# Kernel optimization log

Hardware: AMD Instinct MI355X
Metric: run time of the kernel (lower is better)

## Reference

```python
import jax, jax.numpy as jnp
import numpy as np

N_ITERS = 30  # fixed-iteration surrogate for the data-dependent while-loop power iteration
BN_EPS = 1e-5


def conv1x1(x, w, b):
    # x: [B,C,H,W], w: [O,C], b: [O]
    return jnp.einsum('bchw,oc->bohw', x, w) + b[None, :, None, None]


def bn_relu(x, gamma, beta):
    # training-mode BatchNorm2d (batch statistics over B,H,W per channel) + ReLU
    mean = jnp.mean(x, axis=(0, 2, 3), keepdims=True)
    var = jnp.var(x, axis=(0, 2, 3), keepdims=True)
    xn = (x - mean) * jax.lax.rsqrt(var + BN_EPS)
    return jax.nn.relu(gamma[None, :, None, None] * xn + beta[None, :, None, None])


def power_iteration_u(W, v0):
    # W: [B, N, M]  (N = H*W, M = mid_ch), v0: [B, M]
    # Batched power iteration on W^T W; returns leading left singular vector u: [B, N]
    Ws = jnp.einsum('bnm,bnk->bmk', W, W)  # [B, M, M]

    def step(v, _):
        v = jnp.einsum('bmk,bk->bm', Ws, v)
        v = v / jnp.linalg.norm(v, axis=-1, keepdims=True)
        return v, None

    v, _ = jax.lax.scan(step, v0, None, length=N_ITERS)
    u = jnp.einsum('bnm,bm->bn', W, v)
    u = u / jnp.linalg.norm(u, axis=-1, keepdims=True)
    return u


def setup_inputs() -> dict:
    key = jax.random.key(0)
    B, C, H, W = 32, 64, 128, 128
    M = C // 8  # mid_ch = in_ch // k
    ks = jax.random.split(key, 10)
    he = np.sqrt(2.0 / C).astype(np.float32)
    inp = {
        'x': jax.random.normal(ks[0], (B, C, H, W), dtype=jnp.float32),
        'f_w': jax.random.normal(ks[1], (M, C), dtype=jnp.float32) * he,
        'f_b': jnp.zeros((M,), jnp.float32),
        'f_gamma': jnp.ones((M,), jnp.float32),
        'f_beta': jnp.zeros((M,), jnp.float32),
        'g_w': jax.random.normal(ks[2], (M, C), dtype=jnp.float32) * he,
        'g_b': jnp.zeros((M,), jnp.float32),
        'g_gamma': jnp.ones((M,), jnp.float32),
        'g_beta': jnp.zeros((M,), jnp.float32),
        'h_w': jax.random.normal(ks[3], (M, C), dtype=jnp.float32) * he,
        'h_b': jnp.zeros((M,), jnp.float32),
        'v_w': jax.random.normal(ks[4], (C, M), dtype=jnp.float32) * np.sqrt(2.0 / M).astype(np.float32),
        'v_b': jnp.zeros((C,), jnp.float32),
        'v0f': jax.random.normal(ks[5], (B, M), dtype=jnp.float32),
        'v0g': jax.random.normal(ks[6], (B, M), dtype=jnp.float32),
    }
    return inp


def reference(x, f_w, f_b, f_gamma, f_beta, g_w, g_b, g_gamma, g_beta,
              h_w, h_b, v_w, v_b, v0f, v0g):
    B, C, H, W = x.shape
    M = f_w.shape[0]
    N = H * W
    # f, g: conv1x1 + BN + ReLU; h: conv1x1; all reshaped to [B, N, M]
    fx = bn_relu(conv1x1(x, f_w, f_b), f_gamma, f_beta).reshape(B, M, N).transpose(0, 2, 1)
    gx = bn_relu(conv1x1(x, g_w, g_b), g_gamma, g_beta).reshape(B, M, N).transpose(0, 2, 1)
    hx = conv1x1(x, h_w, h_b).reshape(B, M, N).transpose(0, 2, 1)
    # per-sample leading left singular vectors (batched power iteration)
    uf = power_iteration_u(fx, v0f)  # [B, N]
    ug = power_iteration_u(gx, v0g)  # [B, N]
    # z = u_f @ (u_g^T @ h_x)  -> rank-1 attention, [B, N, M]
    coef = jnp.einsum('bn,bnm->bm', ug, hx)       # [B, M]
    z = uf[:, :, None] * coef[:, None, :]         # [B, N, M]
    z = z.transpose(0, 2, 1).reshape(B, M, H, W)
    z = conv1x1(z, v_w, v_b)
    return z + x
```

## Files before the change

### kernel.cpp

```cpp
#include <hip/hip_runtime.h>

#define BB   32
#define CC   64
#define MM   8
#define NSP  16384
#define CNTF 524288.0f

typedef float f32x4 __attribute__((ext_vector_type(4)));
typedef unsigned int u32x2 __attribute__((ext_vector_type(2)));

#define OFF_FXP_B    0ull
#define OFF_GXP_B    8388608ull
#define OFF_HX_B     16777216ull
#define OFF_PSTATS_B 25165824ull
#define OFF_PWSA_B   (OFF_PSTATS_B + 512ull*32*4)
#define OFF_STATS_B  (OFF_PWSA_B + 32ull*3*8*64*4)

#define AXPY(A, WS, XV) \
    (A).x = fmaf((WS), (XV).x, (A).x); (A).y = fmaf((WS), (XV).y, (A).y); \
    (A).z = fmaf((WS), (XV).z, (A).z); (A).w = fmaf((WS), (XV).w, (A).w);

__device__ __forceinline__ unsigned pk_bf2(float a, float b) {
    unsigned ua = __float_as_uint(a); ua += 0x7FFFu + ((ua >> 16) & 1u);
    unsigned ub = __float_as_uint(b); ub += 0x7FFFu + ((ub >> 16) & 1u);
    return (ua >> 16) | (ub & 0xFFFF0000u);
}
__device__ __forceinline__ float lo16(unsigned u) { return __uint_as_float(u << 16); }
__device__ __forceinline__ float hi16(unsigned u) { return __uint_as_float(u & 0xFFFF0000u); }

__global__ __launch_bounds__(256, 2) void k_conv(const float* __restrict__ x,
        const float* __restrict__ fw, const float* __restrict__ gw,
        const float* __restrict__ hw,
        const float* __restrict__ fb, const float* __restrict__ gb,
        const float* __restrict__ hb, char* __restrict__ wsb) {
    __shared__ float wt[1536];
    __shared__ float sred[4][32];
    for (int i = threadIdx.x; i < 1536; i += 256) {
        int c = i / 24, k = i % 24;
        wt[i] = (k < 8) ? fw[k * 64 + c]
              : (k < 16) ? gw[(k - 8) * 64 + c]
                         : hw[(k - 16) * 64 + c];
    }
    __syncthreads();

    int g  = blockIdx.x * 256 + threadIdx.x;
    int b  = g >> 12;
    int n0 = (g & 4095) * 4;

    const float* xp = x + (size_t)b * CC * NSP + n0;

    float4 af[8], ag[8], ah[8];
#pragma unroll
    for (int m = 0; m < 8; ++m) {
        float bf = fb[m], bg = gb[m], bh = hb[m];
        af[m] = make_float4(bf, bf, bf, bf);
        ag[m] = make_float4(bg, bg, bg, bg);
        ah[m] = make_float4(bh, bh, bh, bh);
    }

#pragma unroll 8
    for (int c = 0; c < 64; ++c) {
        float4 xv = *(const float4*)(xp + (size_t)c * NSP);
        const float4* w4 = (const float4*)(&wt[c * 24]);
        float4 wf0 = w4[0], wf1 = w4[1], wg0 = w4[2], wg1 = w4[3], wh0 = w4[4], wh1 = w4[5];
        AXPY(af[0], wf0.x, xv); AXPY(af[1], wf0.y, xv); AXPY(af[2], wf0.z, xv); AXPY(af[3], wf0.w, xv);
        AXPY(af[4], wf1.x, xv); AXPY(af[5], wf1.y, xv); AXPY(af[6], wf1.z, xv); AXPY(af[7], wf1.w, xv);
        AXPY(ag[0], wg0.x, xv); AXPY(ag[1], wg0.y, xv); AXPY(ag[2], wg0.z, xv); AXPY(ag[3], wg0.w, xv);
        AXPY(ag[4], wg1.x, xv); AXPY(ag[5], wg1.y, xv); AXPY(ag[6], wg1.z, xv); AXPY(ag[7], wg1.w, xv);
        AXPY(ah[0], wh0.x, xv); AXPY(ah[1], wh0.y, xv); AXPY(ah[2], wh0.z, xv); AXPY(ah[3], wh0.w, xv);
        AXPY(ah[4], wh1.x, xv); AXPY(ah[5], wh1.y, xv); AXPY(ah[6], wh1.z, xv); AXPY(ah[7], wh1.w, xv);
    }

    unsigned short* fx16 = (unsigned short*)(wsb + OFF_FXP_B);
    unsigned short* gx16 = (unsigned short*)(wsb + OFF_GXP_B);
    unsigned short* hx16 = (unsigned short*)(wsb + OFF_HX_B);
    size_t base = (size_t)b * MM * NSP + n0;
#pragma unroll
    for (int m = 0; m < 8; ++m) {
        u32x2 pf; pf.x = pk_bf2(af[m].x, af[m].y); pf.y = pk_bf2(af[m].z, af[m].w);
        u32x2 pg; pg.x = pk_bf2(ag[m].x, ag[m].y); pg.y = pk_bf2(ag[m].z, ag[m].w);
        u32x2 ph; ph.x = pk_bf2(ah[m].x, ah[m].y); ph.y = pk_bf2(ah[m].z, ah[m].w);
        *(u32x2*)(fx16 + base + (size_t)m * NSP) = pf;
        *(u32x2*)(gx16 + base + (size_t)m * NSP) = pg;
        *(u32x2*)(hx16 + base + (size_t)m * NSP) = ph;
    }

    int wid = threadIdx.x >> 6, lane = threadIdx.x & 63;
#pragma unroll
    for (int m = 0; m < 8; ++m) {
        float fs = af[m].x + af[m].y + af[m].z + af[m].w;
        float fq = af[m].x * af[m].x + af[m].y * af[m].y + af[m].z * af[m].z + af[m].w * af[m].w;
        float gs = ag[m].x + ag[m].y + ag[m].z + ag[m].w;
        float gq = ag[m].x * ag[m].x + ag[m].y * ag[m].y + ag[m].z * ag[m].z + ag[m].w * ag[m].w;
#pragma unroll
        for (int o = 1; o < 64; o <<= 1) {
            fs += __shfl_xor(fs, o); fq += __shfl_xor(fq, o);
            gs += __shfl_xor(gs, o); gq += __shfl_xor(gq, o);
        }
        if (lane == 0) {
            sred[wid][m] = fs; sred[wid][8 + m] = fq;
            sred[wid][16 + m] = gs; sred[wid][24 + m] = gq;
        }
    }
    __syncthreads();
    if (threadIdx.x < 32) {
        float t = sred[0][threadIdx.x] + sred[1][threadIdx.x]
                + sred[2][threadIdx.x] + sred[3][threadIdx.x];
        ((float*)(wsb + OFF_PSTATS_B))[blockIdx.x * 32 + threadIdx.x] = t;
    }
}

__global__ __launch_bounds__(256) void k_gram(
        const float* __restrict__ fgam, const float* __restrict__ fbet,
        const float* __restrict__ ggam, const float* __restrict__ gbet,
        char* __restrict__ wsb) {
    int bid = blockIdx.x;
    int chunk = bid & 7, which = (bid >> 3) % 3, b = bid / 24;

    __shared__ float sst[8][32];
    __shared__ float stot[32];
    {
        int t32 = threadIdx.x & 31, seg = threadIdx.x >> 5;
        const float* ps = (const float*)(wsb + OFF_PSTATS_B);
        float s = 0.f;
#pragma unroll 8
        for (int i = 0; i < 64; ++i) s += ps[(seg * 64 + i) * 32 + t32];
        sst[seg][t32] = s;
    }
    __syncthreads();
    if (threadIdx.x < 32) {
        float t = 0.f;
#pragma unroll
        for (int w = 0; w < 8; ++w) t += sst[w][threadIdx.x];
        stot[threadIdx.x] = t;
        if (bid == 0) ((float*)(wsb + OFF_STATS_B))[threadIdx.x] = t;
    }
    __syncthreads();

    const float* st  = stot + (which == 0 ? 0 : 16);
    const float* gam = (which == 0) ? fgam : ggam;
    const float* bet = (which == 0) ? fbet : gbet;
    const float inv = 1.f / CNTF;
    float a[8], ccf[8];
#pragma unroll
    for (int m = 0; m < 8; ++m) {
        float mean = st[m] * inv;
        float var  = st[8 + m] * inv - mean * mean;
        float sc   = gam[m] / sqrtf(var + 1e-5f);
        a[m] = sc; ccf[m] = bet[m] - mean * sc;
    }

    const unsigned short* src = (const unsigned short*)
        (wsb + (which == 0 ? OFF_FXP_B : OFF_GXP_B)) + (size_t)b * MM * NSP;
    const unsigned short* hsrc = (const unsigned short*)
        (wsb + OFF_HX_B) + (size_t)b * MM * NSP;

    float acc[64];
#pragma unroll
    for (int j = 0; j < 64; ++j) acc[j] = 0.f;

#pragma unroll
    for (int i = 0; i < 2; ++i) {
        int n = (chunk * 512 + i * 256 + threadIdx.x) * 4;
        float4 vv[8], hh[8];
#pragma unroll
        for (int m = 0; m < 8; ++m) {
            u32x2 u = *(const u32x2*)(src + (size_t)m * NSP + n);
            float4 t;
            t.x = fmaf(a[m], lo16(u.x), ccf[m]); t.x = t.x > 0.f ? t.x : 0.f;
            t.y = fmaf(a[m], hi16(u.x), ccf[m]); t.y = t.y > 0.f ? t.y : 0.f;
            t.z = fmaf(a[m], lo16(u.y), ccf[m]); t.z = t.z > 0.f ? t.z : 0.f;
            t.w = fmaf(a[m], hi16(u.y), ccf[m]); t.w = t.w > 0.f ? t.w : 0.f;
            vv[m] = t;
        }
        if (which == 2) {
#pragma unroll
            for (int m = 0; m < 8; ++m) {
                u32x2 u = *(const u32x2*)(hsrc + (size_t)m * NSP + n);
                hh[m] = make_float4(lo16(u.x), hi16(u.x), lo16(u.y), hi16(u.y));
            }
        } else {
#pragma unroll
            for (int m = 0; m < 8; ++m) hh[m] = vv[m];
        }
#pragma unroll
        for (int m2 = 0; m2 < 8; ++m2)
#pragma unroll
            for (int k = 0; k < 8; ++k) {
                float t = acc[m2 * 8 + k];
                t = fmaf(hh[m2].x, vv[k].x, t);
                t = fmaf(hh[m2].y, vv[k].y, t);
                t = fmaf(hh[m2].z, vv[k].z, t);
                t = fmaf(hh[m2].w, vv[k].w, t);
                acc[m2 * 8 + k] = t;
            }
    }

    int lane = threadIdx.x & 63;
#pragma unroll
    for (int s2 = 0; s2 < 6; ++s2) {
        int half = 32 >> s2;
        int up = (lane >> s2) & 1;
#pragma unroll
        for (int j = 0; j < 32; ++j) {
            if (j >= half) break;
            float send = up ? acc[j] : acc[j + half];
            float recv = __shfl_xor(send, 1 << s2);
            float keep = up ? acc[j + half] : acc[j];
            acc[j] = keep + recv;
        }
    }
    __shared__ float sacc[64];
    if (threadIdx.x < 64) sacc[threadIdx.x] = 0.f;
    __syncthreads();
    int rev = __brev((unsigned)lane) >> 26;
    atomicAdd(&sacc[rev], acc[0]);
    __syncthreads();
    float* pw = (float*)(wsb + OFF_PWSA_B) + (((size_t)b * 3 + which) * 8 + chunk) * 64;
    if (threadIdx.x < 64) pw[threadIdx.x] = sacc[threadIdx.x];
}

__global__ __launch_bounds__(256, 4) void k_out(const float* __restrict__ x,
        const float* __restrict__ fgam, const float* __restrict__ fbet,
        const float* __restrict__ vw, const float* __restrict__ vb,
        const float* __restrict__ v0f, const float* __restrict__ v0g,
        const char* __restrict__ wsb, float* __restrict__ out) {
    int bid = blockIdx.x;
    int b = bid >> 5, sub = bid & 31;
    int tile = sub & 15, ch0 = (sub >> 4) * 32;
    __shared__ float s_vfn[8], s_coef[8], s_w2[64];

    const float* pw = (const float*)(wsb + OFF_PWSA_B) + (size_t)b * 3 * 8 * 64;
    if (threadIdx.x < 16) {
        int grp = threadIdx.x >> 3, m = threadIdx.x & 7;
        float row[8];
#pragma unroll
        for (int k = 0; k < 8; ++k) {
            float s = 0.f;
#pragma unroll
            for (int ch = 0; ch < 8; ++ch) s += pw[(grp * 8 + ch) * 64 + m * 8 + k];
            row[k] = s;
        }
        float v = (grp == 0 ? v0f : v0g)[b * 8 + m];
        for (int it = 0; it < 30; ++it) {
            float t = 0.f;
#pragma unroll
            for (int k = 0; k < 8; ++k) t = fmaf(row[k], __shfl(v, k, 8), t);
            float s = t * t;
            s += __shfl_xor(s, 1, 8); s += __shfl_xor(s, 2, 8); s += __shfl_xor(s, 4, 8);
            v = t / sqrtf(s);
        }
        float t = 0.f;
#pragma unroll
        for (int k = 0; k < 8; ++k) t = fmaf(row[k], __shfl(v, k, 8), t);
        float s = v * t;
        s += __shfl_xor(s, 1, 8); s += __shfl_xor(s, 2, 8); s += __shfl_xor(s, 4, 8);
        float invn = 1.f / sqrtf(s);
        if (grp == 0) {
            s_vfn[m] = v * invn;
        } else {
            float cf = 0.f;
#pragma unroll
            for (int k = 0; k < 8; ++k) {
                float cr = 0.f;
#pragma unroll
                for (int ch = 0; ch < 8; ++ch) cr += pw[(2 * 8 + ch) * 64 + m * 8 + k];
                cf = fmaf(cr, __shfl(v, k, 8), cf);
            }
            s_coef[m] = cf * invn;
        }
    }
    __syncthreads();
    if (threadIdx.x < 64) {
        float acc = 0.f;
#pragma unroll
        for (int k = 0; k < 8; ++k) acc = fmaf(vw[threadIdx.x * 8 + k], s_coef[k], acc);
        s_w2[threadIdx.x] = acc;
    }
    __syncthreads();

    int n0 = tile * 1024 + threadIdx.x * 4;
    const float inv = 1.f / CNTF;
    const float* stats = (const float*)(wsb + OFF_STATS_B);
    const unsigned short* fx16 = (const unsigned short*)(wsb + OFF_FXP_B);

    float uf0 = 0.f, uf1 = 0.f, uf2 = 0.f, uf3 = 0.f;
#pragma unroll
    for (int m = 0; m < 8; ++m) {
        float mean = stats[m] * inv;
        float var  = stats[8 + m] * inv - mean * mean;
        float a    = fgam[m] / sqrtf(var + 1e-5f);
        float cc   = fbet[m] - mean * a;
        float vf   = s_vfn[m];
        u32x2 u = *(const u32x2*)(fx16 + (size_t)(b * 8 + m) * NSP + n0);
        float t0 = fmaf(a, lo16(u.x), cc); t0 = t0 > 0.f ? t0 : 0.f; uf0 = fmaf(vf, t0, uf0);
        float t1 = fmaf(a, hi16(u.x), cc); t1 = t1 > 0.f ? t1 : 0.f; uf1 = fmaf(vf, t1, uf1);
        float t2 = fmaf(a, lo16(u.y), cc); t2 = t2 > 0.f ? t2 : 0.f; uf2 = fmaf(vf, t2, uf2);
        float t3 = fmaf(a, hi16(u.y), cc); t3 = t3 > 0.f ? t3 : 0.f; uf3 = fmaf(vf, t3, uf3);
    }

    const float* xp = x   + (size_t)(b * CC + ch0) * NSP + n0;
    float*       op = out + (size_t)(b * CC + ch0) * NSP + n0;
#pragma unroll 8
    for (int c = 0; c < 32; ++c) {
        float w2c = s_w2[ch0 + c];
        float bc  = vb[ch0 + c];
        float4 xv = *(const float4*)(xp + (size_t)c * NSP);
        f32x4 ov;
        ov.x = fmaf(uf0, w2c, xv.x + bc);
        ov.y = fmaf(uf1, w2c, xv.y + bc);
        ov.z = fmaf(uf2, w2c, xv.z + bc);
        ov.w = fmaf(uf3, w2c, xv.w + bc);
        __builtin_nontemporal_store(ov, (f32x4*)(op + (size_t)c * NSP));
    }
}

extern "C" void kernel_launch(void* const* d_in, const int* in_sizes, int n_in,
                              void* d_out, int out_size, void* d_ws, size_t ws_size,
                              hipStream_t stream) {
    const float* x    = (const float*)d_in[0];
    const float* f_w  = (const float*)d_in[1];
    const float* f_b  = (const float*)d_in[2];
    const float* f_g  = (const float*)d_in[3];
    const float* f_be = (const float*)d_in[4];
    const float* g_w  = (const float*)d_in[5];
    const float* g_b  = (const float*)d_in[6];
    const float* g_g  = (const float*)d_in[7];
    const float* g_be = (const float*)d_in[8];
    const float* h_w  = (const float*)d_in[9];
    const float* h_b  = (const float*)d_in[10];
    const float* v_w  = (const float*)d_in[11];
    const float* v_b  = (const float*)d_in[12];
    const float* v0f  = (const float*)d_in[13];
    const float* v0g  = (const float*)d_in[14];
    char*  wsb = (char*)d_ws;
    float* out = (float*)d_out;

    k_conv<<<512,  256, 0, stream>>>(x, f_w, g_w, h_w, f_b, g_b, h_b, wsb);
    k_gram<<<768,  256, 0, stream>>>(f_g, f_be, g_g, g_be, wsb);
    k_out <<<1024, 256, 0, stream>>>(x, f_g, f_be, v_w, v_b, v0f, v0g, wsb, out);
}
```

Measured before the change: 102.3 us.

## Halve conv per-thread width and move power iteration into separate kernel

Result: slower. 113.1 us (+10.6%).

```diff
diff --git a/kernel.cpp b/kernel.cpp
--- a/kernel.cpp
+++ b/kernel.cpp
@@ -7,18 +7,18 @@
 #define CNTF 524288.0f
 
 typedef float f32x4 __attribute__((ext_vector_type(4)));
+typedef float f32x2 __attribute__((ext_vector_type(2)));
 typedef unsigned int u32x2 __attribute__((ext_vector_type(2)));
 
 #define OFF_FXP_B    0ull
 #define OFF_GXP_B    8388608ull
 #define OFF_HX_B     16777216ull
 #define OFF_PSTATS_B 25165824ull
-#define OFF_PWSA_B   (OFF_PSTATS_B + 512ull*32*4)
+#define OFF_PWSA_B   (OFF_PSTATS_B + 1024ull*32*4)
 #define OFF_STATS_B  (OFF_PWSA_B + 32ull*3*8*64*4)
-
-#define AXPY(A, WS, XV) \
-    (A).x = fmaf((WS), (XV).x, (A).x); (A).y = fmaf((WS), (XV).y, (A).y); \
-    (A).z = fmaf((WS), (XV).z, (A).z); (A).w = fmaf((WS), (XV).w, (A).w);
+#define OFF_COEF_B   (OFF_STATS_B + 32ull*4)
+#define OFF_VFN_B    (OFF_COEF_B + 16ull*4)
+#define OFF_W2_B     (OFF_VFN_B + (unsigned long long)BB*8*4)
 
 __device__ __forceinline__ unsigned pk_bf2(float a, float b) {
     unsigned ua = __float_as_uint(a); ua += 0x7FFFu + ((ua >> 16) & 1u);
@@ -28,7 +28,7 @@
 __device__ __forceinline__ float lo16(unsigned u) { return __uint_as_float(u << 16); }
 __device__ __forceinline__ float hi16(unsigned u) { return __uint_as_float(u & 0xFFFF0000u); }
 
-__global__ __launch_bounds__(256, 2) void k_conv(const float* __restrict__ x,
+__global__ __launch_bounds__(256, 4) void k_conv(const float* __restrict__ x,
         const float* __restrict__ fw, const float* __restrict__ gw,
         const float* __restrict__ hw,
         const float* __restrict__ fb, const float* __restrict__ gb,
@@ -44,31 +44,32 @@
     __syncthreads();
 
     int g  = blockIdx.x * 256 + threadIdx.x;
-    int b  = g >> 12;
-    int n0 = (g & 4095) * 4;
+    int b  = g >> 13;
+    int n0 = (g & 8191) * 2;
 
     const float* xp = x + (size_t)b * CC * NSP + n0;
 
-    float4 af[8], ag[8], ah[8];
-#pragma unroll
-    for (int m = 0; m < 8; ++m) {
-        float bf = fb[m], bg = gb[m], bh = hb[m];
-        af[m] = make_float4(bf, bf, bf, bf);
-        ag[m] = make_float4(bg, bg, bg, bg);
-        ah[m] = make_float4(bh, bh, bh, bh);
+    f32x2 af[8], ag[8], ah[8];
+#pragma unroll
+    for (int m = 0; m < 8; ++m) {
+        af[m].x = af[m].y = fb[m];
+        ag[m].x = ag[m].y = gb[m];
+        ah[m].x = ah[m].y = hb[m];
     }
 
 #pragma unroll 8
     for (int c = 0; c < 64; ++c) {
-        float4 xv = *(const float4*)(xp + (size_t)c * NSP);
+        f32x2 xv = *(const f32x2*)(xp + (size_t)c * NSP);
         const float4* w4 = (const float4*)(&wt[c * 24]);
         float4 wf0 = w4[0], wf1 = w4[1], wg0 = w4[2], wg1 = w4[3], wh0 = w4[4], wh1 = w4[5];
-        AXPY(af[0], wf0.x, xv); AXPY(af[1], wf0.y, xv); AXPY(af[2], wf0.z, xv); AXPY(af[3], wf0.w, xv);
-        AXPY(af[4], wf1.x, xv); AXPY(af[5], wf1.y, xv); AXPY(af[6], wf1.z, xv); AXPY(af[7], wf1.w, xv);
-        AXPY(ag[0], wg0.x, xv); AXPY(ag[1], wg0.y, xv); AXPY(ag[2], wg0.z, xv); AXPY(ag[3], wg0.w, xv);
-        AXPY(ag[4], wg1.x, xv); AXPY(ag[5], wg1.y, xv); AXPY(ag[6], wg1.z, xv); AXPY(ag[7], wg1.w, xv);
-        AXPY(ah[0], wh0.x, xv); AXPY(ah[1], wh0.y, xv); AXPY(ah[2], wh0.z, xv); AXPY(ah[3], wh0.w, xv);
-        AXPY(ah[4], wh1.x, xv); AXPY(ah[5], wh1.y, xv); AXPY(ah[6], wh1.z, xv); AXPY(ah[7], wh1.w, xv);
+#define A2(A, W) (A).x = fmaf((W), xv.x, (A).x); (A).y = fmaf((W), xv.y, (A).y);
+        A2(af[0], wf0.x) A2(af[1], wf0.y) A2(af[2], wf0.z) A2(af[3], wf0.w)
+        A2(af[4], wf1.x) A2(af[5], wf1.y) A2(af[6], wf1.z) A2(af[7], wf1.w)
+        A2(ag[0], wg0.x) A2(ag[1], wg0.y) A2(ag[2], wg0.z) A2(ag[3], wg0.w)
+        A2(ag[4], wg1.x) A2(ag[5], wg1.y) A2(ag[6], wg1.z) A2(ag[7], wg1.w)
+        A2(ah[0], wh0.x) A2(ah[1], wh0.y) A2(ah[2], wh0.z) A2(ah[3], wh0.w)
+        A2(ah[4], wh1.x) A2(ah[5], wh1.y) A2(ah[6], wh1.z) A2(ah[7], wh1.w)
+#undef A2
     }
 
     unsigned short* fx16 = (unsigned short*)(wsb + OFF_FXP_B);
@@ -77,21 +78,18 @@
     size_t base = (size_t)b * MM * NSP + n0;
 #pragma unroll
     for (int m = 0; m < 8; ++m) {
-        u32x2 pf; pf.x = pk_bf2(af[m].x, af[m].y); pf.y = pk_bf2(af[m].z, af[m].w);
-        u32x2 pg; pg.x = pk_bf2(ag[m].x, ag[m].y); pg.y = pk_bf2(ag[m].z, ag[m].w);
-        u32x2 ph; ph.x = pk_bf2(ah[m].x, ah[m].y); ph.y = pk_bf2(ah[m].z, ah[m].w);
-        *(u32x2*)(fx16 + base + (size_t)m * NSP) = pf;
-        *(u32x2*)(gx16 + base + (size_t)m * NSP) = pg;
-        *(u32x2*)(hx16 + base + (size_t)m * NSP) = ph;
+        *(unsigned*)(fx16 + base + (size_t)m * NSP) = pk_bf2(af[m].x, af[m].y);
+        *(unsigned*)(gx16 + base + (size_t)m * NSP) = pk_bf2(ag[m].x, ag[m].y);
+        *(unsigned*)(hx16 + base + (size_t)m * NSP) = pk_bf2(ah[m].x, ah[m].y);
     }
 
     int wid = threadIdx.x >> 6, lane = threadIdx.x & 63;
 #pragma unroll
     for (int m = 0; m < 8; ++m) {
-        float fs = af[m].x + af[m].y + af[m].z + af[m].w;
-        float fq = af[m].x * af[m].x + af[m].y * af[m].y + af[m].z * af[m].z + af[m].w * af[m].w;
-        float gs = ag[m].x + ag[m].y + ag[m].z + ag[m].w;
-        float gq = ag[m].x * ag[m].x + ag[m].y * ag[m].y + ag[m].z * ag[m].z + ag[m].w * ag[m].w;
+        float fs = af[m].x + af[m].y;
+        float fq = af[m].x * af[m].x + af[m].y * af[m].y;
+        float gs = ag[m].x + ag[m].y;
+        float gq = ag[m].x * ag[m].x + ag[m].y * ag[m].y;
 #pragma unroll
         for (int o = 1; o < 64; o <<= 1) {
             fs += __shfl_xor(fs, o); fq += __shfl_xor(fq, o);
@@ -124,7 +122,7 @@
         const float* ps = (const float*)(wsb + OFF_PSTATS_B);
         float s = 0.f;
 #pragma unroll 8
-        for (int i = 0; i < 64; ++i) s += ps[(seg * 64 + i) * 32 + t32];
+        for (int i = 0; i < 128; ++i) s += ps[(seg * 128 + i) * 32 + t32];
         sst[seg][t32] = s;
     }
     __syncthreads();
@@ -220,19 +218,17 @@
     if (threadIdx.x < 64) pw[threadIdx.x] = sacc[threadIdx.x];
 }
 
-__global__ __launch_bounds__(256, 4) void k_out(const float* __restrict__ x,
-        const float* __restrict__ fgam, const float* __restrict__ fbet,
-        const float* __restrict__ vw, const float* __restrict__ vb,
-        const float* __restrict__ v0f, const float* __restrict__ v0g,
-        const char* __restrict__ wsb, float* __restrict__ out) {
-    int bid = blockIdx.x;
-    int b = bid >> 5, sub = bid & 31;
-    int tile = sub & 15, ch0 = (sub >> 4) * 32;
-    __shared__ float s_vfn[8], s_coef[8], s_w2[64];
-
+__global__ void k_power(const float* __restrict__ fgam, const float* __restrict__ fbet,
+                        const float* __restrict__ vw,
+                        const float* __restrict__ v0f, const float* __restrict__ v0g,
+                        char* __restrict__ wsb) {
+    int b = blockIdx.x;
+    int lane = threadIdx.x;
+    __shared__ float coef[8], vfn[8];
     const float* pw = (const float*)(wsb + OFF_PWSA_B) + (size_t)b * 3 * 8 * 64;
-    if (threadIdx.x < 16) {
-        int grp = threadIdx.x >> 3, m = threadIdx.x & 7;
+
+    if (lane < 16) {
+        int grp = lane >> 3, m = lane & 7;
         float row[8];
 #pragma unroll
         for (int k = 0; k < 8; ++k) {
@@ -257,7 +253,7 @@
         s += __shfl_xor(s, 1, 8); s += __shfl_xor(s, 2, 8); s += __shfl_xor(s, 4, 8);
         float invn = 1.f / sqrtf(s);
         if (grp == 0) {
-            s_vfn[m] = v * invn;
+            vfn[m] = v * invn;
         } else {
             float cf = 0.f;
 #pragma unroll
@@ -267,31 +263,53 @@
                 for (int ch = 0; ch < 8; ++ch) cr += pw[(2 * 8 + ch) * 64 + m * 8 + k];
                 cf = fmaf(cr, __shfl(v, k, 8), cf);
             }
-            s_coef[m] = cf * invn;
-        }
-    }
-    __syncthreads();
-    if (threadIdx.x < 64) {
-        float acc = 0.f;
-#pragma unroll
-        for (int k = 0; k < 8; ++k) acc = fmaf(vw[threadIdx.x * 8 + k], s_coef[k], acc);
-        s_w2[threadIdx.x] = acc;
+            coef[m] = cf * invn;
+        }
+    }
+    __syncthreads();
+    {
+        float a2 = 0.f;
+#pragma unroll
+        for (int k = 0; k < 8; ++k) a2 = fmaf(vw[lane * 8 + k], coef[k], a2);
+        ((float*)(wsb + OFF_W2_B))[b * 64 + lane] = a2;
+    }
+    if (lane < 8)
+        ((float*)(wsb + OFF_VFN_B))[b * 8 + lane] = vfn[lane];
+    if (b == 0 && lane < 8) {
+        const float* stats = (const float*)(wsb + OFF_STATS_B);
+        float inv = 1.f / CNTF;
+        float mean = stats[lane] * inv;
+        float var  = stats[8 + lane] * inv - mean * mean;
+        float sc   = fgam[lane] / sqrtf(var + 1e-5f);
+        float* cf = (float*)(wsb + OFF_COEF_B);
+        cf[lane] = sc; cf[8 + lane] = fbet[lane] - mean * sc;
+    }
+}
+
+__global__ __launch_bounds__(256, 4) void k_out(const float* __restrict__ x,
+        const float* __restrict__ vb,
+        const char* __restrict__ wsb, float* __restrict__ out) {
+    int bid = blockIdx.x;
+    int b = bid >> 5, sub = bid & 31;
+    int tile = sub & 15, ch0 = (sub >> 4) * 32;
+    __shared__ float s_vfn[8], s_scf[8], s_off[8], s_w2[64];
+
+    if (threadIdx.x < 64) s_w2[threadIdx.x] = ((const float*)(wsb + OFF_W2_B))[b * 64 + threadIdx.x];
+    if (threadIdx.x < 8) {
+        s_vfn[threadIdx.x] = ((const float*)(wsb + OFF_VFN_B))[b * 8 + threadIdx.x];
+        const float* cf = (const float*)(wsb + OFF_COEF_B);
+        s_scf[threadIdx.x] = cf[threadIdx.x];
+        s_off[threadIdx.x] = cf[8 + threadIdx.x];
     }
     __syncthreads();
 
     int n0 = tile * 1024 + threadIdx.x * 4;
-    const float inv = 1.f / CNTF;
-    const float* stats = (const float*)(wsb + OFF_STATS_B);
     const unsigned short* fx16 = (const unsigned short*)(wsb + OFF_FXP_B);
 
     float uf0 = 0.f, uf1 = 0.f, uf2 = 0.f, uf3 = 0.f;
 #pragma unroll
     for (int m = 0; m < 8; ++m) {
-        float mean = stats[m] * inv;
-        float var  = stats[8 + m] * inv - mean * mean;
-        float a    = fgam[m] / sqrtf(var + 1e-5f);
-        float cc   = fbet[m] - mean * a;
-        float vf   = s_vfn[m];
+        float a  = s_scf[m], cc = s_off[m], vf = s_vfn[m];
         u32x2 u = *(const u32x2*)(fx16 + (size_t)(b * 8 + m) * NSP + n0);
         float t0 = fmaf(a, lo16(u.x), cc); t0 = t0 > 0.f ? t0 : 0.f; uf0 = fmaf(vf, t0, uf0);
         float t1 = fmaf(a, hi16(u.x), cc); t1 = t1 > 0.f ? t1 : 0.f; uf1 = fmaf(vf, t1, uf1);
@@ -336,7 +354,8 @@
     char*  wsb = (char*)d_ws;
     float* out = (float*)d_out;
 
-    k_conv<<<512,  256, 0, stream>>>(x, f_w, g_w, h_w, f_b, g_b, h_b, wsb);
-    k_gram<<<768,  256, 0, stream>>>(f_g, f_be, g_g, g_be, wsb);
-    k_out <<<1024, 256, 0, stream>>>(x, f_g, f_be, v_w, v_b, v0f, v0g, wsb, out);
-}
+    k_conv <<<1024, 256, 0, stream>>>(x, f_w, g_w, h_w, f_b, g_b, h_b, wsb);
+    k_gram <<<768,  256, 0, stream>>>(f_g, f_be, g_g, g_be, wsb);
+    k_power<<<32,   64,  0, stream>>>(f_g, f_be, v_w, v0f, v0g, wsb);
+    k_out  <<<1024, 256, 0, stream>>>(x, v_b, wsb, out);
+}
```
